# Kernel optimization log

Hardware: AMD Instinct MI355X
Metric: run time of the kernel (lower is better)

The kernel has to match this reference:

```python
import jax, jax.numpy as jnp
import numpy as np

WEIGHT = 0.1
N_BINS = 64
EPS = 1e-08  # fp32: max(base_eps, 1e-8)


def setup_inputs() -> dict:
    key = jax.random.key(0)
    k1, k2 = jax.random.split(key)
    pred = jax.random.normal(k1, (16, 1, 512, 512), dtype=jnp.float32)
    target = jax.random.normal(k2, (16, 1, 512, 512), dtype=jnp.float32)
    return {"pred": pred, "target": target}


def _soft_hist(x_norm, bin_centers, bin_width):
    # x_norm: [B, N]; bin_centers: [n_bins]
    # Gaussian kernel density -> sum over N -> [B, n_bins]
    diff = x_norm[:, :, None] - bin_centers[None, None, :]  # [B, N, n_bins]
    kern = jnp.exp(-(diff ** 2) / (2.0 * bin_width ** 2))
    return kern.sum(axis=1)


def reference(pred, target):
    B = pred.shape[0]
    pred_flat = pred.reshape(B, -1)
    target_flat = target.reshape(B, -1)

    vmin = target_flat.min(axis=-1, keepdims=True)
    vmax = target_flat.max(axis=-1, keepdims=True)

    bin_edges = jnp.linspace(0.0, 1.0, N_BINS + 1, dtype=pred.dtype)
    bin_centers = (bin_edges[:-1] + bin_edges[1:]) / 2
    bin_width = bin_edges[1] - bin_edges[0]

    denom = vmax - vmin + EPS
    pred_norm = (pred_flat - vmin) / denom
    target_norm = (target_flat - vmin) / denom

    pred_hist = _soft_hist(pred_norm, bin_centers, bin_width)      # [B, n_bins]
    target_hist = _soft_hist(target_norm, bin_centers, bin_width)  # [B, n_bins]

    pred_prob = pred_hist / (pred_hist.sum(axis=-1, keepdims=True) + EPS)
    target_prob = target_hist / (target_hist.sum(axis=-1, keepdims=True) + EPS)

    kl = target_prob * (jnp.log(target_prob + EPS) - jnp.log(pred_prob + EPS))
    return WEIGHT * kl.sum(axis=-1).mean()
```

## Files before the change

kernel.cpp:

```cpp
#include <hip/hip_runtime.h>
#include <math.h>

#define NB    16
#define NPB   (512*512)
#define NBINS 64
#define MMB   64
#define CB    64
#define EPSF  1e-8f
#define QF    0.84932180517f
#define L2E   1.44269504089f
#define LN2   0.69314718056f
#define K16   1.12535175e-7f
#define K16I  8886110.5f


typedef float v2f __attribute__((ext_vector_type(2)));


__global__ __launch_bounds__(256) void minmax_k(const float4* __restrict__ tgt,
                                                float* __restrict__ mmn,
                                                float* __restrict__ mmx,
                                                float* __restrict__ hist) {
    const int batch = blockIdx.x / MMB, sub = blockIdx.x % MMB;
    if (sub == 0 && threadIdx.x < 128) {
        const int tens = threadIdx.x >> 6, lane = threadIdx.x & 63;
        hist[(tens * NB + batch) * NBINS + lane] = 0.0f;
    }

    const int F4 = NPB / 4 / MMB;
    const float4* p = tgt + (size_t)batch * (NPB / 4) + (size_t)sub * F4;
    float mn = 3.4e38f, mx = -3.4e38f;
    #pragma unroll
    for (int i = 0; i < F4 / 256; ++i) {
        float4 v = p[i * 256 + threadIdx.x];
        mn = fminf(mn, fminf(fminf(v.x, v.y), fminf(v.z, v.w)));
        mx = fmaxf(mx, fmaxf(fmaxf(v.x, v.y), fmaxf(v.z, v.w)));
    }
    #pragma unroll
    for (int o = 1; o < 64; o <<= 1) {
        mn = fminf(mn, __shfl_xor(mn, o));
        mx = fmaxf(mx, __shfl_xor(mx, o));
    }
    __shared__ float smn[4], smx[4];
    const int wave = threadIdx.x >> 6, lane = threadIdx.x & 63;
    if (lane == 0) { smn[wave] = mn; smx[wave] = mx; }
    __syncthreads();
    if (threadIdx.x == 0) {
        mmn[blockIdx.x] = fminf(fminf(smn[0], smn[1]), fminf(smn[2], smn[3]));
        mmx[blockIdx.x] = fmaxf(fmaxf(smx[0], smx[1]), fmaxf(smx[2], smx[3]));
    }
}

__device__ __forceinline__ void point32(float xin, float s64, float bk8,
                                        v2f* __restrict__ acc2) {
    const float C1 = 0.60653065971f,    C2 = 0.13533528324f,
                C3 = 0.01110899654f,    C4 = 3.35462627903e-4f,
                C5 = 3.72665317208e-6f, C6 = 1.52299797447e-8f,
                C7 = 2.28973484833e-11f, C8 = 1.26641655490e-14f;
    const v2f c1 = {C1, C1}, c2 = {C2, C2}, c3 = {C3, C3}, c4 = {C4, C4},
              c5 = {C5, C5}, c6 = {C6, C6}, c7 = {C7, C7}, c8 = {C8, C8};
    float d   = fmaf(xin, s64, bk8);
    float dc  = __builtin_amdgcn_fmed3f(d, -30.0f, 46.0f);
    float x   = dc * L2E;
    float r   = __builtin_amdgcn_exp2f(x);
    float ri  = __builtin_amdgcn_exp2f(-x);
    float t1  = dc * QF;
    float A1  = __builtin_amdgcn_exp2f(-(t1 * t1));
    float t2  = fmaf(dc, QF, -16.0f * QF);
    float A2  = __builtin_amdgcn_exp2f(-(t2 * t2));
    v2f RR = {r,  r  * K16};
    v2f RI = {ri, ri * K16I};
    v2f TS = {A1, A2};
    v2f UV = TS;
    acc2[8] += TS;
    TS *= RR; acc2[9]  = __builtin_elementwise_fma(TS, c1, acc2[9]);
    TS *= RR; acc2[10] = __builtin_elementwise_fma(TS, c2, acc2[10]);
    TS *= RR; acc2[11] = __builtin_elementwise_fma(TS, c3, acc2[11]);
    TS *= RR; acc2[12] = __builtin_elementwise_fma(TS, c4, acc2[12]);
    TS *= RR; acc2[13] = __builtin_elementwise_fma(TS, c5, acc2[13]);
    TS *= RR; acc2[14] = __builtin_elementwise_fma(TS, c6, acc2[14]);
    TS *= RR; acc2[15] = __builtin_elementwise_fma(TS, c7, acc2[15]);
    UV *= RI; acc2[7]  = __builtin_elementwise_fma(UV, c1, acc2[7]);
    UV *= RI; acc2[6]  = __builtin_elementwise_fma(UV, c2, acc2[6]);
    UV *= RI; acc2[5]  = __builtin_elementwise_fma(UV, c3, acc2[5]);
    UV *= RI; acc2[4]  = __builtin_elementwise_fma(UV, c4, acc2[4]);
    UV *= RI; acc2[3]  = __builtin_elementwise_fma(UV, c5, acc2[3]);
    UV *= RI; acc2[2]  = __builtin_elementwise_fma(UV, c6, acc2[2]);
    UV *= RI; acc2[1]  = __builtin_elementwise_fma(UV, c7, acc2[1]);
    UV *= RI; acc2[0]  = __builtin_elementwise_fma(UV, c8, acc2[0]);
}

__global__ __launch_bounds__(256, 4) void hist_k(const float4* __restrict__ pred,
                                                 const float4* __restrict__ tgt,
                                                 const float* __restrict__ mmn,
                                                 const float* __restrict__ mmx,
                                                 float* __restrict__ hist) {
    const int blk   = blockIdx.x;
    const int tens  = blk & 1;
    const int batch = (blk >> 1) & (NB - 1);
    const int chunk = blk >> 5;
    const int wave  = threadIdx.x >> 6, lane = threadIdx.x & 63;
    const int kwb   = 32 * (wave & 1);
    const int pair  = wave >> 1;

    const int F4C = NPB / 4 / CB;
    const int F4H = F4C / 2;
    const float4* __restrict__ src = (tens ? tgt : pred)
        + (size_t)batch * (NPB / 4) + (size_t)chunk * F4C + (size_t)pair * F4H;

    float4 v = src[lane];

    float vmin = mmn[batch * MMB + lane];
    float vmax = mmx[batch * MMB + lane];
    #pragma unroll
    for (int o = 1; o < 64; o <<= 1) {
        vmin = fminf(vmin, __shfl_xor(vmin, o));
        vmax = fmaxf(vmax, __shfl_xor(vmax, o));
    }
    const float s64 = 64.0f / (vmax - vmin + EPSF);
    const float bk8 = fmaf(-vmin, s64, -0.5f) - (float)(kwb + 8);

    v2f acc2[16];
    #pragma unroll
    for (int k = 0; k < 16; ++k) acc2[k] = (v2f){0.0f, 0.0f};

    const int NIT = F4H / 64;
    #pragma unroll 1
    for (int it = 0; it < NIT; ++it) {
        float4 vn = src[(it < NIT - 1 ? (it + 1) * 64 : 0) + lane];
        point32(v.x, s64, bk8, acc2);
        point32(v.y, s64, bk8, acc2);
        point32(v.z, s64, bk8, acc2);
        point32(v.w, s64, bk8, acc2);
        v = vn;
    }

    float val[32];
    #pragma unroll
    for (int k = 0; k < 16; ++k) { val[k] = acc2[k].x; val[16 + k] = acc2[k].y; }
    #pragma unroll
    for (int s = 0; s < 5; ++s) {
        const int o = 1 << s;
        const bool b = (lane >> s) & 1;
        #pragma unroll
        for (int p = 0; p < (16 >> s); ++p) {
            float lo = val[2 * p], hi = val[2 * p + 1];
            float vk = b ? hi : lo;
            float vo = b ? lo : hi;
            val[p] = vk + __shfl_xor(vo, o);
        }
    }
    float tot = val[0] + __shfl_xor(val[0], 32);
    if (lane < 32)
        unsafeAtomicAdd(&hist[(tens * NB + batch) * NBINS + kwb + lane], tot);
}

__global__ __launch_bounds__(256) void final_k(const float* __restrict__ hist,
                                               float* __restrict__ out) {
    const int lane = threadIdx.x & 63, wave = threadIdx.x >> 6;
    __shared__ float wacc[4];
    float a = 0.0f;
    for (int b = wave; b < NB; b += 4) {
        float hp = hist[b * NBINS + lane];
        float ht = hist[(NB + b) * NBINS + lane];
        float sp = hp, st = ht;
        #pragma unroll
        for (int o = 1; o < 64; o <<= 1) {
            sp += __shfl_xor(sp, o);
            st += __shfl_xor(st, o);
        }
        float pp = hp / (sp + EPSF);
        float pt = ht / (st + EPSF);
        float term = pt * ((__builtin_amdgcn_logf(pt + EPSF)
                          - __builtin_amdgcn_logf(pp + EPSF)) * LN2);
        #pragma unroll
        for (int o = 1; o < 64; o <<= 1) term += __shfl_xor(term, o);
        a += term;
    }
    if (lane == 0) wacc[wave] = a;
    __syncthreads();
    if (threadIdx.x == 0)
        out[0] = 0.1f * (wacc[0] + wacc[1] + wacc[2] + wacc[3]) / (float)NB;
}

extern "C" void kernel_launch(void* const* d_in, const int* in_sizes, int n_in,
                              void* d_out, int out_size, void* d_ws, size_t ws_size,
                              hipStream_t stream) {
    const float* pred = (const float*)d_in[0];
    const float* tgt  = (const float*)d_in[1];
    float* mmn  = (float*)d_ws;
    float* mmx  = mmn + NB * MMB;
    float* hist = mmx + NB * MMB;
    float* out  = (float*)d_out;

    minmax_k<<<NB * MMB, 256, 0, stream>>>((const float4*)tgt, mmn, mmx, hist);
    hist_k  <<<2 * NB * CB, 256, 0, stream>>>((const float4*)pred, (const float4*)tgt,
                                              mmn, mmx, hist);
    final_k <<<1, 256, 0, stream>>>(hist, out);
}
```

Baseline: 103.2 us.

## Have each wave compute all 64 bins per point instead of 32

Each wave now covers all 64 bins for its points, using four anchor Gaussians and two packed accumulator sets, rather than splitting the bins across wave pairs. This shares the per-point exp2 of r and 1/r across twice as many bins and halves the number of times each point is loaded and normalized per bin set. In exchange it doubles accumulator registers, lowers the launch-bounds occupancy hint from 4 to 2, and raises the d clamp range to 78.

```diff
diff --git a/kernel.cpp b/kernel.cpp
--- a/kernel.cpp
+++ b/kernel.cpp
@@ -12,6 +12,10 @@
 #define LN2   0.69314718056f
 #define K16   1.12535175e-7f
 #define K16I  8886110.5f
+#define K32   1.26641655e-14f
+#define K32I  7.8962960e13f
+#define K48   1.42516408e-21f
+#define K48I  7.01673591e20f
 
 
 typedef float v2f __attribute__((ext_vector_type(2)));
@@ -51,8 +55,9 @@
     }
 }
 
-__device__ __forceinline__ void point32(float xin, float s64, float bk8,
-                                        v2f* __restrict__ acc2) {
+__device__ __forceinline__ void point64(float xin, float s64, float bk8,
+                                        v2f* __restrict__ accA,
+                                        v2f* __restrict__ accB) {
     const float C1 = 0.60653065971f,    C2 = 0.13533528324f,
                 C3 = 0.01110899654f,    C4 = 3.35462627903e-4f,
                 C5 = 3.72665317208e-6f, C6 = 1.52299797447e-8f,
@@ -60,7 +65,7 @@
     const v2f c1 = {C1, C1}, c2 = {C2, C2}, c3 = {C3, C3}, c4 = {C4, C4},
               c5 = {C5, C5}, c6 = {C6, C6}, c7 = {C7, C7}, c8 = {C8, C8};
     float d   = fmaf(xin, s64, bk8);
-    float dc  = __builtin_amdgcn_fmed3f(d, -30.0f, 46.0f);
+    float dc  = __builtin_amdgcn_fmed3f(d, -30.0f, 78.0f);
     float x   = dc * L2E;
     float r   = __builtin_amdgcn_exp2f(x);
     float ri  = __builtin_amdgcn_exp2f(-x);
@@ -68,29 +73,50 @@
     float A1  = __builtin_amdgcn_exp2f(-(t1 * t1));
     float t2  = fmaf(dc, QF, -16.0f * QF);
     float A2  = __builtin_amdgcn_exp2f(-(t2 * t2));
-    v2f RR = {r,  r  * K16};
-    v2f RI = {ri, ri * K16I};
-    v2f TS = {A1, A2};
-    v2f UV = TS;
-    acc2[8] += TS;
-    TS *= RR; acc2[9]  = __builtin_elementwise_fma(TS, c1, acc2[9]);
-    TS *= RR; acc2[10] = __builtin_elementwise_fma(TS, c2, acc2[10]);
-    TS *= RR; acc2[11] = __builtin_elementwise_fma(TS, c3, acc2[11]);
-    TS *= RR; acc2[12] = __builtin_elementwise_fma(TS, c4, acc2[12]);
-    TS *= RR; acc2[13] = __builtin_elementwise_fma(TS, c5, acc2[13]);
-    TS *= RR; acc2[14] = __builtin_elementwise_fma(TS, c6, acc2[14]);
-    TS *= RR; acc2[15] = __builtin_elementwise_fma(TS, c7, acc2[15]);
-    UV *= RI; acc2[7]  = __builtin_elementwise_fma(UV, c1, acc2[7]);
-    UV *= RI; acc2[6]  = __builtin_elementwise_fma(UV, c2, acc2[6]);
-    UV *= RI; acc2[5]  = __builtin_elementwise_fma(UV, c3, acc2[5]);
-    UV *= RI; acc2[4]  = __builtin_elementwise_fma(UV, c4, acc2[4]);
-    UV *= RI; acc2[3]  = __builtin_elementwise_fma(UV, c5, acc2[3]);
-    UV *= RI; acc2[2]  = __builtin_elementwise_fma(UV, c6, acc2[2]);
-    UV *= RI; acc2[1]  = __builtin_elementwise_fma(UV, c7, acc2[1]);
-    UV *= RI; acc2[0]  = __builtin_elementwise_fma(UV, c8, acc2[0]);
-}
-
-__global__ __launch_bounds__(256, 4) void hist_k(const float4* __restrict__ pred,
+    float t3  = fmaf(dc, QF, -32.0f * QF);
+    float A3  = __builtin_amdgcn_exp2f(-(t3 * t3));
+    float t4  = fmaf(dc, QF, -48.0f * QF);
+    float A4  = __builtin_amdgcn_exp2f(-(t4 * t4));
+    v2f RRa = {r,        r * K16};
+    v2f RRb = {r * K32,  r * K48};
+    v2f RIa = {ri,       ri * K16I};
+    v2f RIb = {ri * K32I, ri * K48I};
+    v2f TA = {A1, A2}, TB = {A3, A4};
+    v2f UA = TA, UB = TB;
+    accA[8] += TA;  accB[8] += TB;
+    TA *= RRa; accA[9]  = __builtin_elementwise_fma(TA, c1, accA[9]);
+    TB *= RRb; accB[9]  = __builtin_elementwise_fma(TB, c1, accB[9]);
+    TA *= RRa; accA[10] = __builtin_elementwise_fma(TA, c2, accA[10]);
+    TB *= RRb; accB[10] = __builtin_elementwise_fma(TB, c2, accB[10]);
+    TA *= RRa; accA[11] = __builtin_elementwise_fma(TA, c3, accA[11]);
+    TB *= RRb; accB[11] = __builtin_elementwise_fma(TB, c3, accB[11]);
+    TA *= RRa; accA[12] = __builtin_elementwise_fma(TA, c4, accA[12]);
+    TB *= RRb; accB[12] = __builtin_elementwise_fma(TB, c4, accB[12]);
+    TA *= RRa; accA[13] = __builtin_elementwise_fma(TA, c5, accA[13]);
+    TB *= RRb; accB[13] = __builtin_elementwise_fma(TB, c5, accB[13]);
+    TA *= RRa; accA[14] = __builtin_elementwise_fma(TA, c6, accA[14]);
+    TB *= RRb; accB[14] = __builtin_elementwise_fma(TB, c6, accB[14]);
+    TA *= RRa; accA[15] = __builtin_elementwise_fma(TA, c7, accA[15]);
+    TB *= RRb; accB[15] = __builtin_elementwise_fma(TB, c7, accB[15]);
+    UA *= RIa; accA[7]  = __builtin_elementwise_fma(UA, c1, accA[7]);
+    UB *= RIb; accB[7]  = __builtin_elementwise_fma(UB, c1, accB[7]);
+    UA *= RIa; accA[6]  = __builtin_elementwise_fma(UA, c2, accA[6]);
+    UB *= RIb; accB[6]  = __builtin_elementwise_fma(UB, c2, accB[6]);
+    UA *= RIa; accA[5]  = __builtin_elementwise_fma(UA, c3, accA[5]);
+    UB *= RIb; accB[5]  = __builtin_elementwise_fma(UB, c3, accB[5]);
+    UA *= RIa; accA[4]  = __builtin_elementwise_fma(UA, c4, accA[4]);
+    UB *= RIb; accB[4]  = __builtin_elementwise_fma(UB, c4, accB[4]);
+    UA *= RIa; accA[3]  = __builtin_elementwise_fma(UA, c5, accA[3]);
+    UB *= RIb; accB[3]  = __builtin_elementwise_fma(UB, c5, accB[3]);
+    UA *= RIa; accA[2]  = __builtin_elementwise_fma(UA, c6, accA[2]);
+    UB *= RIb; accB[2]  = __builtin_elementwise_fma(UB, c6, accB[2]);
+    UA *= RIa; accA[1]  = __builtin_elementwise_fma(UA, c7, accA[1]);
+    UB *= RIb; accB[1]  = __builtin_elementwise_fma(UB, c7, accB[1]);
+    UA *= RIa; accA[0]  = __builtin_elementwise_fma(UA, c8, accA[0]);
+    UB *= RIb; accB[0]  = __builtin_elementwise_fma(UB, c8, accB[0]);
+}
+
+__global__ __launch_bounds__(256, 2) void hist_k(const float4* __restrict__ pred,
                                                  const float4* __restrict__ tgt,
                                                  const float* __restrict__ mmn,
                                                  const float* __restrict__ mmx,
@@ -100,13 +126,11 @@
     const int batch = (blk >> 1) & (NB - 1);
     const int chunk = blk >> 5;
     const int wave  = threadIdx.x >> 6, lane = threadIdx.x & 63;
-    const int kwb   = 32 * (wave & 1);
-    const int pair  = wave >> 1;
 
     const int F4C = NPB / 4 / CB;
-    const int F4H = F4C / 2;
+    const int F4Q = F4C / 4;
     const float4* __restrict__ src = (tens ? tgt : pred)
-        + (size_t)batch * (NPB / 4) + (size_t)chunk * F4C + (size_t)pair * F4H;
+        + (size_t)batch * (NPB / 4) + (size_t)chunk * F4C + (size_t)wave * F4Q;
 
     float4 v = src[lane];
 
@@ -118,41 +142,47 @@
         vmax = fmaxf(vmax, __shfl_xor(vmax, o));
     }
     const float s64 = 64.0f / (vmax - vmin + EPSF);
-    const float bk8 = fmaf(-vmin, s64, -0.5f) - (float)(kwb + 8);
-
-    v2f acc2[16];
-    #pragma unroll
-    for (int k = 0; k < 16; ++k) acc2[k] = (v2f){0.0f, 0.0f};
-
-    const int NIT = F4H / 64;
+    const float bk8 = fmaf(-vmin, s64, -0.5f) - 8.0f;
+
+    v2f accA[16], accB[16];
+    #pragma unroll
+    for (int k = 0; k < 16; ++k) {
+        accA[k] = (v2f){0.0f, 0.0f};
+        accB[k] = (v2f){0.0f, 0.0f};
+    }
+
+    const int NIT = F4Q / 64;
     #pragma unroll 1
     for (int it = 0; it < NIT; ++it) {
         float4 vn = src[(it < NIT - 1 ? (it + 1) * 64 : 0) + lane];
-        point32(v.x, s64, bk8, acc2);
-        point32(v.y, s64, bk8, acc2);
-        point32(v.z, s64, bk8, acc2);
-        point32(v.w, s64, bk8, acc2);
+        point64(v.x, s64, bk8, accA, accB);
+        point64(v.y, s64, bk8, accA, accB);
+        point64(v.z, s64, bk8, accA, accB);
+        point64(v.w, s64, bk8, accA, accB);
         v = vn;
     }
 
-    float val[32];
-    #pragma unroll
-    for (int k = 0; k < 16; ++k) { val[k] = acc2[k].x; val[16 + k] = acc2[k].y; }
-    #pragma unroll
-    for (int s = 0; s < 5; ++s) {
+    float val[64];
+    #pragma unroll
+    for (int k = 0; k < 16; ++k) {
+        val[k]      = accA[k].x;
+        val[16 + k] = accA[k].y;
+        val[32 + k] = accB[k].x;
+        val[48 + k] = accB[k].y;
+    }
+    #pragma unroll
+    for (int s = 0; s < 6; ++s) {
         const int o = 1 << s;
         const bool b = (lane >> s) & 1;
         #pragma unroll
-        for (int p = 0; p < (16 >> s); ++p) {
+        for (int p = 0; p < (32 >> s); ++p) {
             float lo = val[2 * p], hi = val[2 * p + 1];
             float vk = b ? hi : lo;
             float vo = b ? lo : hi;
             val[p] = vk + __shfl_xor(vo, o);
         }
     }
-    float tot = val[0] + __shfl_xor(val[0], 32);
-    if (lane < 32)
-        unsafeAtomicAdd(&hist[(tens * NB + batch) * NBINS + kwb + lane], tot);
+    unsafeAtomicAdd(&hist[(tens * NB + batch) * NBINS + lane], val[0]);
 }
 
 __global__ __launch_bounds__(256) void final_k(const float* __restrict__ hist,
```

Result: no change. 102.8 us (-0.4%).
